# Performance work log

Hardware: AMD Instinct MI355X
Metric: run time of the kernel (lower is better)

Reference implementation:

```python
import jax, jax.numpy as jnp
import numpy as np

D_MODEL = 1024
N_HEAD = 16
HEAD_DIM = D_MODEL // N_HEAD
D_FF = 4096
N_EXPERTS = 4
EPS = 1e-05


def _layer_norm(x, gamma, beta):
    mu = jnp.mean(x, axis=-1, keepdims=True)
    var = jnp.mean((x - mu) ** 2, axis=-1, keepdims=True)
    return (x - mu) / jnp.sqrt(var + EPS) * gamma + beta


def setup_inputs() -> dict:
    key = jax.random.key(0)
    ks = jax.random.split(key, 20)
    f32 = jnp.float32
    sc = 1.0 / np.sqrt(D_MODEL)
    scf = 1.0 / np.sqrt(D_FF)
    return {
        "src": jax.random.normal(ks[0], (4, 512, D_MODEL), f32),
        "Wq": jax.random.normal(ks[1], (D_MODEL, D_MODEL), f32) * sc,
        "bq": jnp.zeros((D_MODEL,), f32),
        "Wk": jax.random.normal(ks[2], (D_MODEL, D_MODEL), f32) * sc,
        "bk": jnp.zeros((D_MODEL,), f32),
        "Wv": jax.random.normal(ks[3], (D_MODEL, D_MODEL), f32) * sc,
        "bv": jnp.zeros((D_MODEL,), f32),
        "Wo": jax.random.normal(ks[4], (D_MODEL, D_MODEL), f32) * sc,
        "bo": jnp.zeros((D_MODEL,), f32),
        "router_w": jax.random.normal(ks[5], (D_MODEL, 1), f32) * 0.05,
        "router_b": jnp.zeros((1,), f32),
        "W1": jax.random.normal(ks[6], (N_EXPERTS, D_MODEL, D_FF), f32) * sc,
        "b1": jnp.zeros((N_EXPERTS, D_FF), f32),
        "W2": jax.random.normal(ks[7], (N_EXPERTS, D_FF, D_MODEL), f32) * scf,
        "b2": jnp.zeros((N_EXPERTS, D_MODEL), f32),
        "ln1_g": jnp.ones((D_MODEL,), f32),
        "ln1_b": jnp.zeros((D_MODEL,), f32),
        "ln2_g": jnp.ones((D_MODEL,), f32),
        "ln2_b": jnp.zeros((D_MODEL,), f32),
    }


def reference(src, Wq, bq, Wk, bk, Wv, bv, Wo, bo, router_w, router_b,
              W1, b1, W2, b2, ln1_g, ln1_b, ln2_g, ln2_b):
    B, T, _ = src.shape
    # --- self attention ---
    q = (src @ Wq + bq).reshape(B, T, N_HEAD, HEAD_DIM)
    k = (src @ Wk + bk).reshape(B, T, N_HEAD, HEAD_DIM)
    v = (src @ Wv + bv).reshape(B, T, N_HEAD, HEAD_DIM)
    scale = HEAD_DIM ** -0.5
    scores = jnp.einsum('bqhd,bkhd->bhqk', q, k) * scale
    probs = jax.nn.softmax(scores, axis=-1)
    attn = jnp.einsum('bhqk,bkhd->bqhd', probs, v).reshape(B, T, D_MODEL)
    attn = attn @ Wo + bo
    x = _layer_norm(src + attn, ln1_g, ln1_b)
    # --- hash-routed single-expert MoE FFN ---
    keys = (x @ router_w + router_b)[..., 0]           # [B, T]
    expert_idx = jnp.remainder(jnp.floor(keys).astype(jnp.int32), N_EXPERTS)
    ff_out = jnp.zeros_like(x)
    for e in range(N_EXPERTS):
        h = jax.nn.relu(x @ W1[e] + b1[e])             # [B, T, D_FF]
        y = h @ W2[e] + b2[e]                          # [B, T, D_MODEL]
        ff_out = ff_out + jnp.where((expert_idx == e)[..., None], y, 0.0)
    return _layer_norm(x + ff_out, ln2_g, ln2_b)
```

## Files before the change

kernel.cpp:

```cpp
#include <hip/hip_runtime.h>
#include <hip/hip_bf16.h>
#include <stdint.h>

typedef unsigned short u16;
typedef __attribute__((ext_vector_type(8))) short s8v;
typedef __attribute__((ext_vector_type(4))) float f4v;

#define DEVI static __device__ __forceinline__

DEVI u16 f2bf(float x) {
  union { float f; unsigned u; } a; a.f = x;
  return (u16)((a.u + 0x7fffu + ((a.u >> 16) & 1u)) >> 16);
}
DEVI float bf2f(u16 h) {
  union { float f; unsigned u; } a; a.u = ((unsigned)h) << 16; return a.f;
}
DEVI float wred_add(float s) {
#pragma unroll
  for (int o = 32; o; o >>= 1) s += __shfl_xor(s, o, 64);
  return s;
}
DEVI f4v mfma16(s8v a, s8v b, f4v c) {
  return __builtin_amdgcn_mfma_f32_16x16x32_bf16(a, b, c, 0, 0, 0);
}

DEVI int rho(int j) { return ((j & 12) << 1) | (j & 3) | ((j >> 4) << 2); }

DEVI void gload16(const u16* gp, u16* lp) {
  __builtin_amdgcn_global_load_lds(
      (const __attribute__((address_space(1))) uint32_t*)gp,
      (__attribute__((address_space(3))) uint32_t*)lp, 16, 0, 0);
}

DEVI s8v ldfrag_sw(const u16* base, int r, int lg) {
  int off = ((r >> 4) << 9) + ((r & 15) << 5) + ((lg ^ ((r >> 1) & 3)) << 3);
  return *(const s8v*)(base + off);
}

template<bool LO>
DEVI void tsplit_body(const float* __restrict__ in, u16* __restrict__ outH, u16* __restrict__ outL,
                      int cc, int rr, int R, int C, float (*t)[132], int id) {
#pragma unroll
  for (int i = 0; i < 4; ++i) {
    int slot = i * 256 + id;
    int r = slot >> 5, c4 = slot & 31;
    float4 v = *(const float4*)&in[(long long)(rr + r) * C + cc + c4 * 4];
    *(float4*)&t[r + (r >> 2)][c4 * 4] = v;
  }
  __syncthreads();
#pragma unroll
  for (int i = 0; i < 4; ++i) {
    int slot = i * 256 + id;
    int j = slot >> 3, gs = slot & 7;
    int s0 = 5 * gs;
    float v0 = t[s0 + 0][j], v1 = t[s0 + 1][j], v2 = t[s0 + 2][j], v3 = t[s0 + 3][j];
    long long o = (long long)(cc + j) * R + rr + 8 * (gs & 3) + 4 * (gs >> 2);
    ushort4 hv;
    hv.x = f2bf(v0); hv.y = f2bf(v1); hv.z = f2bf(v2); hv.w = f2bf(v3);
    *(ushort4*)&outH[o] = hv;
    if (LO) {
      ushort4 lv;
      lv.x = f2bf(v0 - bf2f(hv.x)); lv.y = f2bf(v1 - bf2f(hv.y));
      lv.z = f2bf(v2 - bf2f(hv.z)); lv.w = f2bf(v3 - bf2f(hv.w));
      *(ushort4*)&outL[o] = lv;
    }
  }
}

__global__ __launch_bounds__(256) void prep1_k(const float* __restrict__ src,
    const float* __restrict__ Wq, const float* __restrict__ Wk,
    const float* __restrict__ Wv, const float* __restrict__ Wo,
    const float* __restrict__ bq, const float* __restrict__ bk, const float* __restrict__ bv,
    u16* __restrict__ srcH, u16* __restrict__ srcL,
    u16* __restrict__ WqkvTh, u16* __restrict__ WqkvTl,
    u16* __restrict__ WoTh, u16* __restrict__ WoTl, float* __restrict__ bqkv) {
  __shared__ float tbuf[39][132];
  const int bid = blockIdx.x, tid = threadIdx.x;
  if (bid < 2048) {
    int i = bid * 256 + tid;
    float4 v = ((const float4*)src)[i];
    ushort4 hv, lv;
    hv.x = f2bf(v.x); lv.x = f2bf(v.x - bf2f(hv.x));
    hv.y = f2bf(v.y); lv.y = f2bf(v.y - bf2f(hv.y));
    hv.z = f2bf(v.z); lv.z = f2bf(v.z - bf2f(hv.z));
    hv.w = f2bf(v.w); lv.w = f2bf(v.w - bf2f(hv.w));
    int t = i & 7, blk = i >> 3;
    int si = blk * 8 + ((t & 3) << 1) + (t >> 2);
    ((ushort4*)srcH)[si] = hv;
    ((ushort4*)srcL)[si] = lv;
  } else if (bid < 3072) {
    int t = bid - 2048;
    int wsel = t >> 8, tb = t & 255;
    const float* in = wsel == 0 ? Wq : wsel == 1 ? Wk : wsel == 2 ? Wv : Wo;
    u16* oh = wsel < 3 ? WqkvTh + wsel * 1024 * 1024 : WoTh;
    u16* ol = wsel < 3 ? WqkvTl + wsel * 1024 * 1024 : WoTl;
    tsplit_body<true>(in, oh, ol, (tb & 7) * 128, (tb >> 3) * 32, 1024, 1024, tbuf, tid);
  } else {
    int i = (bid - 3072) * 256 + tid;
    bqkv[i] = i < 1024 ? bq[i] : (i < 2048 ? bk[i - 1024] : bv[i - 2048]);
  }
}

__global__ __launch_bounds__(256) void prep2_k(const float* __restrict__ W1, const float* __restrict__ W2,
                                               u16* __restrict__ W1T, u16* __restrict__ W2T) {
  __shared__ float tbuf[39][132];
  const int bid = blockIdx.x, tid = threadIdx.x;
  if (bid < 4096) {
    int bx = bid & 31, by = (bid >> 5) & 31, bz = bid >> 10;
    tsplit_body<false>(W1 + (long long)bz * 1024 * 4096, W1T + (long long)bz * 4096 * 1024, nullptr,
                       bx * 128, by * 32, 1024, 4096, tbuf, tid);
  } else {
    int t = bid - 4096;
    int bx = t & 7, by = (t >> 3) & 127, bz = t >> 10;
    tsplit_body<false>(W2 + (long long)bz * 4096 * 1024, W2T + (long long)bz * 1024 * 4096, nullptr,
                       bx * 128, by * 32, 4096, 1024, tbuf, tid);
  }
}

__global__ __launch_bounds__(256) void transpose_pair_k(const u16* __restrict__ inH, const u16* __restrict__ inL,
                                                        u16* __restrict__ oH, u16* __restrict__ oL) {
  __shared__ u16 th[32][40], tl[32][40];
  const int b = blockIdx.z;
  const int dd = blockIdx.x * 32;
  const int tt = blockIdx.y * 32;
  const int id = threadIdx.y * 32 + threadIdx.x;
  const int rr = id >> 3, g = id & 7;
  const int rg = 8 * (g & 3) + 4 * (g >> 2);
  const int64_t ibase = ((int64_t)(b * 512 + tt)) * 3072 + 2048 + dd;
  ushort4 hv = *(const ushort4*)&inH[ibase + (int64_t)rr * 3072 + rg];
  ushort4 lv = *(const ushort4*)&inL[ibase + (int64_t)rr * 3072 + rg];
  *(ushort4*)&th[rr][4 * g] = hv;
  *(ushort4*)&tl[rr][4 * g] = lv;
  __syncthreads();
  const int j = rr;
  ushort4 ho, lo;
  ho.x = th[4 * g + 0][j]; ho.y = th[4 * g + 1][j]; ho.z = th[4 * g + 2][j]; ho.w = th[4 * g + 3][j];
  lo.x = tl[4 * g + 0][j]; lo.y = tl[4 * g + 1][j]; lo.z = tl[4 * g + 2][j]; lo.w = tl[4 * g + 3][j];
  const int64_t obase = ((int64_t)b * 1024 + dd + j) * 512 + tt + rg;
  *(ushort4*)&oH[obase] = ho;
  *(ushort4*)&oL[obase] = lo;
}

__global__ __launch_bounds__(512, 2) void attn_sm_k(const u16* __restrict__ qkvH,
                                                    const u16* __restrict__ qkvL,
                                                    u16* __restrict__ probs) {
  __shared__ __align__(16) u16 sK[2][16384];
  __shared__ __align__(16) float smax[128][4];
  __shared__ __align__(16) float ssum[128][4];
  const int tid = threadIdx.x;
  const int w = tid >> 6, lane = tid & 63;
  const int wq = w >> 2, wt = w & 3;
  const int lr = lane & 15, lg = lane >> 4;
  const int bx = blockIdx.x, bh = blockIdx.y;
  const int64_t tokBase = (int64_t)(bh >> 4) * 512;
  const int h = bh & 15;
  const int qcol = h * 64, kcol = 1024 + h * 64;
  const int srow = lane >> 2;
  const int sG = (lane & 3) ^ ((lane >> 3) & 3);

#pragma unroll
  for (int c = 0; c < 8; ++c) {
    int s = c * 8 + w;
    int ks = s >> 5, rb = s & 31;
    int64_t go = (tokBase + rb * 16 + srow) * 3072 + kcol + ks * 32 + sG * 8;
    gload16(qkvH + go, &sK[ks][rb * 512]);
  }
  __syncthreads();

  f4v acc[4][8];
#pragma unroll
  for (int mi = 0; mi < 4; ++mi)
#pragma unroll
    for (int ni = 0; ni < 8; ++ni) acc[mi][ni] = f4v{0.f, 0.f, 0.f, 0.f};

#pragma unroll
  for (int ks = 0; ks < 2; ++ks) {
    s8v ah[4], al[4];
#pragma unroll
    for (int mi = 0; mi < 4; ++mi) {
      int64_t tok = tokBase + bx * 128 + wq * 64 + mi * 16 + lr;
      const u16* p = qkvH + tok * 3072 + qcol + ks * 32 + lg * 8;
      ah[mi] = *(const s8v*)p;
      al[mi] = *(const s8v*)(qkvL + (p - qkvH));
    }
#pragma unroll
    for (int ni = 0; ni < 8; ++ni) {
      int r = wt * 128 + ni * 16 + lr;
      s8v bh_ = ldfrag_sw(&sK[ks][0], r, lg);
      s8v bl_ = *(const s8v*)(qkvL + (tokBase + r) * 3072 + kcol + ks * 32 + lg * 8);
#pragma unroll
      for (int mi = 0; mi < 4; ++mi) {
        acc[mi][ni] = mfma16(ah[mi], bh_, acc[mi][ni]);
        acc[mi][ni] = mfma16(ah[mi], bl_, acc[mi][ni]);
        acc[mi][ni] = mfma16(al[mi], bh_, acc[mi][ni]);
      }
    }
  }

#pragma unroll
  for (int mi = 0; mi < 4; ++mi)
#pragma unroll
    for (int ni = 0; ni < 8; ++ni) {
      acc[mi][ni][0] *= 0.125f; acc[mi][ni][1] *= 0.125f;
      acc[mi][ni][2] *= 0.125f; acc[mi][ni][3] *= 0.125f;
    }

  float rm[4][4];
#pragma unroll
  for (int mi = 0; mi < 4; ++mi)
#pragma unroll
    for (int j = 0; j < 4; ++j) {
      float m = acc[mi][0][j];
#pragma unroll
      for (int ni = 1; ni < 8; ++ni) m = fmaxf(m, acc[mi][ni][j]);
#pragma unroll
      for (int o = 1; o < 16; o <<= 1) m = fmaxf(m, __shfl_xor(m, o, 64));
      rm[mi][j] = m;
    }
  if (lr == 0) {
#pragma unroll
    for (int mi = 0; mi < 4; ++mi)
#pragma unroll
      for (int j = 0; j < 4; ++j)
        smax[wq * 64 + mi * 16 + lg * 4 + j][wt] = rm[mi][j];
  }
  __syncthreads();
  float mrow[4][4];
#pragma unroll
  for (int mi = 0; mi < 4; ++mi)
#pragma unroll
    for (int j = 0; j < 4; ++j) {
      float4 t4 = *(const float4*)&smax[wq * 64 + mi * 16 + lg * 4 + j][0];
      mrow[mi][j] = fmaxf(fmaxf(t4.x, t4.y), fmaxf(t4.z, t4.w));
    }

  float rs_[4][4];
#pragma unroll
  for (int mi = 0; mi < 4; ++mi)
#pragma unroll
    for (int j = 0; j < 4; ++j) {
      float s = 0.f;
#pragma unroll
      for (int ni = 0; ni < 8; ++ni) {
        float e = expf(acc[mi][ni][j] - mrow[mi][j]);
        acc[mi][ni][j] = e;
        s += e;
      }
#pragma unroll
      for (int o = 1; o < 16; o <<= 1) s += __shfl_xor(s, o, 64);
      rs_[mi][j] = s;
    }
  if (lr == 0) {
#pragma unroll
    for (int mi = 0; mi < 4; ++mi)
#pragma unroll
      for (int j = 0; j < 4; ++j)
        ssum[wq * 64 + mi * 16 + lg * 4 + j][wt] = rs_[mi][j];
  }
  __syncthreads();

#pragma unroll
  for (int mi = 0; mi < 4; ++mi)
#pragma unroll
    for (int j = 0; j < 4; ++j) {
      int row = wq * 64 + mi * 16 + lg * 4 + j;
      float4 t4 = *(const float4*)&ssum[row][0];
      float inv = 1.f / (((t4.x + t4.y) + t4.z) + t4.w);
      u16* rp = probs + ((int64_t)bh * 512 + bx * 128 + row) * 1024;
#pragma unroll
      for (int ni = 0; ni < 8; ++ni) {
        int tcol = wt * 128 + ni * 16 + lr;
        int cs = (tcol & ~31) | rho(tcol & 31);
        float p = acc[mi][ni][j] * inv;
        u16 hv = f2bf(p);
        rp[cs] = hv;
        rp[512 + cs] = f2bf(p - bf2f(hv));
      }
    }
}

struct GemmArgs {
  const u16* Ah; const u16* Al; int lda;
  const u16* Bh; const u16* Bl; int ldb;
  float* C; u16* Ch; u16* Cl; int ldc;
  const float* bias;
  int K;
  int Z2;
  int64_t aZ1, aZ2, bZ1, bZ2, cZ1, cZ2;
  const int* ofs;
  int64_t bStrE; int biasStrE;
  int NX, NY, YG;
};

template<int BM, int BN, bool SPLIT, int EPI, bool PN, int MINW, bool SWZ>
__global__ __launch_bounds__(256, MINW) void gemm_k(GemmArgs g) {
  constexpr int ASZ = BM * 32, BSZ = BN * 32;
  constexpr int AN = SPLIT ? 2 * ASZ : ASZ;
  constexpr int BNT = SPLIT ? 2 * BSZ : BSZ;
  constexpr int nA = BM / 16, nB = BN / 16;
  constexpr int nAt = SPLIT ? 2 * nA : nA;
  constexpr int TOT = nAt + (SPLIT ? 2 * nB : nB);
  static_assert(TOT % 4 == 0, "chunk count must divide across 4 waves");
  constexpr int NLOAD = TOT / 4;
  __shared__ __align__(16) u16 sA[2][AN];
  __shared__ __align__(16) u16 sB[2][BNT];

  const int tid = threadIdx.x;
  int bx, by, bz;
  if (SWZ) {
    const int nwg = gridDim.x;
    int wg = (blockIdx.x & 7) * (nwg >> 3) + (blockIdx.x >> 3);
    int byl = wg % g.YG; int t = wg / g.YG;
    bx = t % g.NX; t /= g.NX;
    const int nyg = g.NY / g.YG;
    by = (t % nyg) * g.YG + byl;
    bz = t / nyg;
  } else {
    bx = blockIdx.x; by = blockIdx.y; bz = blockIdx.z;
  }

  const u16* Ah = g.Ah; const u16* Al = g.Al;
  const u16* Bh = g.Bh; const u16* Bl = g.Bl;
  int64_t cOff = 0;
  if (g.Z2 > 0) {
    int z1 = bz / g.Z2, z2 = bz % g.Z2;
    int64_t ao = (int64_t)z1 * g.aZ1 + (int64_t)z2 * g.aZ2;
    int64_t bo = (int64_t)z1 * g.bZ1 + (int64_t)z2 * g.bZ2;
    Ah += ao; Bh += bo;
    if (SPLIT) { Al += ao; Bl += bo; }
    cOff = (int64_t)z1 * g.cZ1 + (int64_t)z2 * g.cZ2;
  }
  const int row0 = bx * BM;
  const int col0 = by * BN;
  const float* bias = g.bias;
  if (g.ofs) {
    if (row0 >= g.ofs[4]) return;
    int e = 0;
    while (e < 3 && row0 >= g.ofs[e + 1]) ++e;
    Bh += (int64_t)e * g.bStrE;
    if (bias) bias += (int64_t)e * g.biasStrE;
  }

  const int w = tid >> 6, lane = tid & 63;
  const int wr = w >> 1, wc = w & 1;
  const int lr = lane & 15, lg = lane >> 4;
  constexpr int FM = BM / 32, FN = BN / 32;

  const int srow = lane >> 2;
  const int sG = (lane & 3) ^ ((lane >> 3) & 3);

  auto stage = [&](int b, int kt) {
#pragma unroll
    for (int c = 0; c < NLOAD; ++c) {
      int s = c * 4 + w;
      if (s < nA) {
        int64_t go = (int64_t)(row0 + s * 16 + srow) * g.lda + kt + sG * 8;
        gload16(Ah + go, &sA[b][s * 512]);
      } else if (SPLIT && s < 2 * nA) {
        int ch = s - nA;
        int64_t go = (int64_t)(row0 + ch * 16 + srow) * g.lda + kt + sG * 8;
        gload16(Al + go, &sA[b][ASZ + ch * 512]);
      } else if (s < nAt + nB) {
        int ch = s - nAt;
        int64_t go = (int64_t)(col0 + ch * 16 + srow) * g.ldb + kt + sG * 8;
        gload16(Bh + go, &sB[b][ch * 512]);
      } else {
        int ch = s - nAt - nB;
        int64_t go = (int64_t)(col0 + ch * 16 + srow) * g.ldb + kt + sG * 8;
        gload16(Bl + go, &sB[b][BSZ + ch * 512]);
      }
    }
  };

  f4v acc[FM][FN];
#pragma unroll
  for (int i = 0; i < FM; ++i)
#pragma unroll
    for (int j = 0; j < FN; ++j) acc[i][j] = f4v{0.f, 0.f, 0.f, 0.f};

  s8v a0[FM], b0[FN], al0[SPLIT ? FM : 1], bl0[SPLIT ? FN : 1];
  s8v a1[FM], b1[FN], al1[SPLIT ? FM : 1], bl1[SPLIT ? FN : 1];

  auto rdfrags = [&](int buf, auto& af, auto& bf, auto& afl, auto& bfl) {
#pragma unroll
    for (int mi = 0; mi < FM; ++mi) {
      int r = wr * (BM / 2) + mi * 16 + lr;
      af[mi] = ldfrag_sw(&sA[buf][0], r, lg);
      if (SPLIT) afl[mi] = ldfrag_sw(&sA[buf][ASZ], r, lg);
    }
#pragma unroll
    for (int ni = 0; ni < FN; ++ni) {
      int r = wc * (BN / 2) + ni * 16 + lr;
      bf[ni] = ldfrag_sw(&sB[buf][0], r, lg);
      if (SPLIT) bfl[ni] = ldfrag_sw(&sB[buf][BSZ], r, lg);
    }
  };

  const int nt = g.K >> 5;

  stage(0, 0);
  stage(1, 32);
  asm volatile("s_waitcnt vmcnt(%0)" :: "n"(NLOAD) : "memory");
  __builtin_amdgcn_sched_barrier(0);
  __builtin_amdgcn_s_barrier();
  rdfrags(0, a0, b0, al0, bl0);

  auto body = [&](int t, auto& cA, auto& cB, auto& cAl, auto& cBl,
                  auto& nA_, auto& nB_, auto& nAl_, auto& nBl_) {
    asm volatile("s_waitcnt lgkmcnt(0)" ::: "memory");
    __builtin_amdgcn_sched_barrier(0);
    __builtin_amdgcn_s_barrier();
    if (t + 2 < nt) stage(t & 1, (t + 2) << 5);
    if (t + 1 < nt) {
      if (t + 2 < nt)
        asm volatile("s_waitcnt vmcnt(%0)" :: "n"(NLOAD) : "memory");
      else
        asm volatile("s_waitcnt vmcnt(0)" ::: "memory");
      __builtin_amdgcn_sched_barrier(0);
      __builtin_amdgcn_s_barrier();
      rdfrags((t + 1) & 1, nA_, nB_, nAl_, nBl_);
    }
    __builtin_amdgcn_sched_barrier(0);
    __builtin_amdgcn_s_setprio(1);
#pragma unroll
    for (int mi = 0; mi < FM; ++mi)
#pragma unroll
      for (int ni = 0; ni < FN; ++ni) {
        acc[mi][ni] = mfma16(cA[mi], cB[ni], acc[mi][ni]);
        if (SPLIT) {
          acc[mi][ni] = mfma16(cA[mi], cBl[ni], acc[mi][ni]);
          acc[mi][ni] = mfma16(cAl[mi], cB[ni], acc[mi][ni]);
        }
      }
    __builtin_amdgcn_s_setprio(0);
  };

  for (int t = 0; t < nt; t += 2) {
    body(t,     a0, b0, al0, bl0, a1, b1, al1, bl1);
    body(t + 1, a1, b1, al1, bl1, a0, b0, al0, bl0);
  }

#pragma unroll
  for (int mi = 0; mi < FM; ++mi) {
    int rbase = row0 + wr * (BM / 2) + mi * 16 + lg * 4;
#pragma unroll
    for (int ni = 0; ni < FN; ++ni) {
      int c = col0 + wc * (BN / 2) + ni * 16 + lr;
      int cs = PN ? ((c & ~31) | rho(c & 31)) : c;
      float bv = bias ? bias[c] : 0.f;
#pragma unroll
      for (int j = 0; j < 4; ++j) {
        int r = rbase + j;
        float v = acc[mi][ni][j] + bv;
        if (EPI == 0) {
          g.C[cOff + (int64_t)r * g.ldc + cs] = v;
        } else if (EPI == 1) {
          u16 h = f2bf(v);
          int64_t o = cOff + (int64_t)r * g.ldc + cs;
          g.Ch[o] = h;
          g.Cl[o] = f2bf(v - bf2f(h));
        } else {
          v = v > 0.f ? v : 0.f;
          g.Ch[cOff + (int64_t)r * g.ldc + cs] = f2bf(v);
        }
      }
    }
  }
}

__global__ __launch_bounds__(256) void ln_router_k(const float* __restrict__ a, const float* __restrict__ b,
                                                   const float* __restrict__ gm, const float* __restrict__ bt,
                                                   const float* __restrict__ rw, const float* __restrict__ rb,
                                                   float* __restrict__ out, int* __restrict__ eidx) {
  __shared__ float sm[4];
  const int r = blockIdx.x, tid = threadIdx.x;
  const int w = tid >> 6, lane = tid & 63;
  float4 va = ((const float4*)(a + (int64_t)r * 1024))[tid];
  float4 vb = ((const float4*)(b + (int64_t)r * 1024))[tid];
  float x0 = va.x + vb.x, x1 = va.y + vb.y, x2 = va.z + vb.z, x3 = va.w + vb.w;
  float s = wred_add(x0 + x1 + x2 + x3);
  if (lane == 0) sm[w] = s;
  __syncthreads();
  float mu = (sm[0] + sm[1] + sm[2] + sm[3]) * (1.f / 1024.f);
  float d0 = x0 - mu, d1 = x1 - mu, d2 = x2 - mu, d3 = x3 - mu;
  float q = wred_add(d0 * d0 + d1 * d1 + d2 * d2 + d3 * d3);
  __syncthreads();
  if (lane == 0) sm[w] = q;
  __syncthreads();
  float var = (sm[0] + sm[1] + sm[2] + sm[3]) * (1.f / 1024.f);
  float rs = 1.f / sqrtf(var + 1e-5f);
  float4 g4 = ((const float4*)gm)[tid];
  float4 b4 = ((const float4*)bt)[tid];
  float4 o;
  o.x = d0 * rs * g4.x + b4.x;
  o.y = d1 * rs * g4.y + b4.y;
  o.z = d2 * rs * g4.z + b4.z;
  o.w = d3 * rs * g4.w + b4.w;
  ((float4*)(out + (int64_t)r * 1024))[tid] = o;
  float4 w4 = ((const float4*)rw)[tid];
  float p = o.x * w4.x + o.y * w4.y + o.z * w4.z + o.w * w4.w;
  p = wred_add(p);
  __syncthreads();
  if (lane == 0) sm[w] = p;
  __syncthreads();
  if (tid == 0) {
    float key = (sm[0] + sm[1] + sm[2] + sm[3]) + rb[0];
    eidx[r] = (int)floorf(key) & 3;
  }
}

__global__ __launch_bounds__(256) void reduce_ln_k(const float* __restrict__ part, const int* __restrict__ rowsrc,
                                                   const int* __restrict__ ofs, const float* __restrict__ b2,
                                                   const float* __restrict__ xb, const float* __restrict__ gm,
                                                   const float* __restrict__ bt, float* __restrict__ out) {
  __shared__ float sm[4];
  const int r = blockIdx.x;
  if (r >= ofs[4]) return;
  const int s = rowsrc[r];
  if (s < 0) return;
  int e = 0;
  while (e < 3 && r >= ofs[e + 1]) ++e;
  const int tid = threadIdx.x, w = tid >> 6, lane = tid & 63;
  const int64_t RN = 2560ll * 1024;
  float4 v0 = ((const float4*)(part + 0 * RN + (int64_t)r * 1024))[tid];
  float4 v1 = ((const float4*)(part + 1 * RN + (int64_t)r * 1024))[tid];
  float4 v2 = ((const float4*)(part + 2 * RN + (int64_t)r * 1024))[tid];
  float4 v3 = ((const float4*)(part + 3 * RN + (int64_t)r * 1024))[tid];
  float4 bb = ((const float4*)(b2 + (int64_t)e * 1024))[tid];
  float4 va = ((const float4*)(xb + (int64_t)s * 1024))[tid];
  float y0 = ((v0.x + v1.x) + v2.x) + v3.x + bb.x;
  float y1 = ((v0.y + v1.y) + v2.y) + v3.y + bb.y;
  float y2 = ((v0.z + v1.z) + v2.z) + v3.z + bb.z;
  float y3 = ((v0.w + v1.w) + v2.w) + v3.w + bb.w;
  float x0 = va.x + y0, x1 = va.y + y1, x2 = va.z + y2, x3 = va.w + y3;
  float sum = wred_add(x0 + x1 + x2 + x3);
  if (lane == 0) sm[w] = sum;
  __syncthreads();
  float mu = (sm[0] + sm[1] + sm[2] + sm[3]) * (1.f / 1024.f);
  float d0 = x0 - mu, d1 = x1 - mu, d2 = x2 - mu, d3 = x3 - mu;
  float q = wred_add(d0 * d0 + d1 * d1 + d2 * d2 + d3 * d3);
  __syncthreads();
  if (lane == 0) sm[w] = q;
  __syncthreads();
  float var = (sm[0] + sm[1] + sm[2] + sm[3]) * (1.f / 1024.f);
  float rs = 1.f / sqrtf(var + 1e-5f);
  float4 g4 = ((const float4*)gm)[tid];
  float4 b4 = ((const float4*)bt)[tid];
  float4 o;
  o.x = d0 * rs * g4.x + b4.x;
  o.y = d1 * rs * g4.y + b4.y;
  o.z = d2 * rs * g4.z + b4.z;
  o.w = d3 * rs * g4.w + b4.w;
  ((float4*)(out + (int64_t)s * 1024))[tid] = o;
}

__global__ __launch_bounds__(256) void compact_k(const int* __restrict__ eidx,
                                                 int* __restrict__ rowsrc, int* __restrict__ ofs) {
  __shared__ unsigned long long sc[256];
  __shared__ int soff[5];
  const int tid = threadIdx.x;
  int myE[8];
  unsigned long long c = 0;
#pragma unroll
  for (int i = 0; i < 8; ++i) {
    int e = eidx[tid * 8 + i];
    myE[i] = e;
    c += 1ull << (e * 16);
  }
  sc[tid] = c;
  __syncthreads();
  for (int o = 1; o < 256; o <<= 1) {
    unsigned long long v = (tid >= o) ? sc[tid - o] : 0ull;
    __syncthreads();
    sc[tid] += v;
    __syncthreads();
  }
  unsigned long long incl = sc[tid], tot = sc[255];
  unsigned long long excl = incl - c;
  if (tid == 0) {
    int off = 0;
    for (int e = 0; e < 4; ++e) {
      soff[e] = off;
      int cnt = (int)((tot >> (e * 16)) & 0xffff);
      off += (cnt + 127) & ~127;
    }
    soff[4] = off;
    for (int e = 0; e < 5; ++e) ofs[e] = soff[e];
  }
  __syncthreads();
  for (int r = tid; r < 2560; r += 256) rowsrc[r] = -1;
  __threadfence_block();
  __syncthreads();
  int rank[4];
#pragma unroll
  for (int e = 0; e < 4; ++e) rank[e] = (int)((excl >> (e * 16)) & 0xffff);
#pragma unroll
  for (int i = 0; i < 8; ++i) {
    int e = myE[i];
    rowsrc[soff[e] + rank[e]] = tid * 8 + i;
    rank[e]++;
  }
}

__global__ __launch_bounds__(256) void gather_k(const float* __restrict__ x, const int* __restrict__ rowsrc,
                                                const int* __restrict__ ofs, u16* __restrict__ xg) {
  int r = blockIdx.x;
  if (r >= ofs[4]) return;
  int s = rowsrc[r];
  int c = threadIdx.x;
  float4 v = (s >= 0) ? ((const float4*)(x + (int64_t)s * 1024))[c] : float4{0.f, 0.f, 0.f, 0.f};
  ushort4 o;
  o.x = f2bf(v.x); o.y = f2bf(v.y); o.z = f2bf(v.z); o.w = f2bf(v.w);
  int t = c & 7, blk = c >> 3;
  int si = blk * 8 + ((t & 3) << 1) + (t >> 2);
  ((ushort4*)(xg + (int64_t)r * 1024))[si] = o;
}

extern "C" void kernel_launch(void* const* d_in, const int* in_sizes, int n_in,
                              void* d_out, int out_size, void* d_ws, size_t ws_size,
                              hipStream_t stream) {
  const float* src = (const float*)d_in[0];
  const float* Wq  = (const float*)d_in[1];
  const float* bq  = (const float*)d_in[2];
  const float* Wk  = (const float*)d_in[3];
  const float* bk  = (const float*)d_in[4];
  const float* Wv  = (const float*)d_in[5];
  const float* bv  = (const float*)d_in[6];
  const float* Wo  = (const float*)d_in[7];
  const float* bo  = (const float*)d_in[8];
  const float* rw  = (const float*)d_in[9];
  const float* rb  = (const float*)d_in[10];
  const float* W1  = (const float*)d_in[11];
  const float* b1  = (const float*)d_in[12];
  const float* W2  = (const float*)d_in[13];
  const float* b2  = (const float*)d_in[14];
  const float* g1  = (const float*)d_in[15];
  const float* be1 = (const float*)d_in[16];
  const float* g2  = (const float*)d_in[17];
  const float* be2 = (const float*)d_in[18];
  float* out = (float*)d_out;

  char* base = (char*)d_ws;
  size_t off = 0;
  auto alloc = [&](size_t bytes) -> char* {
    char* p = base + off;
    off += (bytes + 255) & ~(size_t)255;
    return p;
  };
  const size_t MB = 1ull << 20;
  u16* srcH = (u16*)alloc(4 * MB);
  u16* srcL = (u16*)alloc(4 * MB);
  u16* WqkvTh = (u16*)alloc(6 * MB);
  u16* WqkvTl = (u16*)alloc(6 * MB);
  u16* WoTh = (u16*)alloc(2 * MB);
  u16* WoTl = (u16*)alloc(2 * MB);
  float* bqkv = (float*)alloc(16 * 1024);
  u16* qkvH = (u16*)alloc(12 * MB);
  u16* qkvL = (u16*)alloc(12 * MB);
  u16* hbuf = (u16*)qkvH;
  u16* vTH = (u16*)alloc(4 * MB); u16* vTL = (u16*)alloc(4 * MB);
  float* scores = (float*)alloc(64 * MB);
  u16* W1T = (u16*)scores;
  u16* W2T = (u16*)scores + 16ull * 1024 * 1024;
  u16* attnH = (u16*)alloc(4 * MB); u16* attnL = (u16*)alloc(4 * MB);
  u16* xg = (u16*)attnH;
  float* woOut = (float*)alloc(8 * MB);
  float* xbuf = (float*)alloc(8 * MB);
  float* partials = (float*)alloc(40 * MB);
  int* eidx   = (int*)alloc(2048 * 4);
  int* rowsrc = (int*)alloc(2560 * 4);
  int* ofs    = (int*)alloc(32);
  (void)ws_size; (void)in_sizes; (void)n_in; (void)out_size;

  dim3 tb(32, 8);

  prep1_k<<<3084, 256, 0, stream>>>(src, Wq, Wk, Wv, Wo, bq, bk, bv,
                                    srcH, srcL, WqkvTh, WqkvTl, WoTh, WoTl, bqkv);

  {
    GemmArgs g{};
    g.Ah = srcH; g.Al = srcL; g.lda = 1024;
    g.Bh = WqkvTh; g.Bl = WqkvTl; g.ldb = 1024;
    g.Ch = qkvH; g.Cl = qkvL; g.ldc = 3072;
    g.bias = bqkv; g.K = 1024; g.Z2 = 0;
    g.NX = 16; g.NY = 32; g.YG = 8;
    gemm_k<128, 96, true, 1, true, 2, true><<<dim3(512), 256, 0, stream>>>(g);
  }
  transpose_pair_k<<<dim3(32, 16, 4), tb, 0, stream>>>(qkvH, qkvL, vTH, vTL);

  attn_sm_k<<<dim3(4, 64), 512, 0, stream>>>(qkvH, qkvL, (u16*)scores);

  {
    GemmArgs g{};
    g.Ah = (const u16*)scores; g.Al = (const u16*)scores + 512; g.lda = 1024;
    g.Bh = vTH; g.Bl = vTL; g.ldb = 512;
    g.Ch = attnH; g.Cl = attnL; g.ldc = 1024;
    g.K = 512; g.Z2 = 16;
    g.aZ1 = 16ll * 512 * 1024; g.aZ2 = 512ll * 1024;
    g.bZ1 = 1024ll * 512;      g.bZ2 = 64ll * 512;
    g.cZ1 = 512ll * 1024;      g.cZ2 = 64;
    gemm_k<64, 64, true, 1, true, 3, false><<<dim3(8, 1, 64), 256, 0, stream>>>(g);
  }
  {
    GemmArgs g{};
    g.Ah = attnH; g.Al = attnL; g.lda = 1024;
    g.Bh = WoTh; g.Bl = WoTl; g.ldb = 1024;
    g.C = woOut; g.ldc = 1024;
    g.bias = bo; g.K = 1024; g.Z2 = 0;
    gemm_k<64, 64, true, 0, false, 3, false><<<dim3(32, 16, 1), 256, 0, stream>>>(g);
  }
  ln_router_k<<<2048, 256, 0, stream>>>(src, woOut, g1, be1, rw, rb, xbuf, eidx);

  compact_k<<<1, 256, 0, stream>>>(eidx, rowsrc, ofs);
  gather_k<<<2560, 256, 0, stream>>>(xbuf, rowsrc, ofs, xg);

  prep2_k<<<8192, 256, 0, stream>>>(W1, W2, W1T, W2T);

  {
    GemmArgs g{};
    g.Ah = xg; g.lda = 1024;
    g.Bh = W1T; g.ldb = 1024;
    g.Ch = hbuf; g.ldc = 4096;
    g.bias = b1; g.biasStrE = 4096;
    g.K = 1024; g.Z2 = 0;
    g.ofs = ofs; g.bStrE = 4096ll * 1024;
    g.NX = 20; g.NY = 32; g.YG = 16;
    gemm_k<128, 128, false, 2, true, 3, true><<<dim3(640), 256, 0, stream>>>(g);
  }
  {
    GemmArgs g{};
    g.Ah = hbuf; g.lda = 4096;
    g.Bh = W2T; g.ldb = 4096;
    g.C = partials; g.ldc = 1024;
    g.bias = nullptr;
    g.K = 1024; g.Z2 = 4;
    g.aZ1 = 0; g.aZ2 = 1024;
    g.bZ1 = 0; g.bZ2 = 1024;
    g.cZ1 = 0; g.cZ2 = 2560ll * 1024;
    g.ofs = ofs; g.bStrE = 4096ll * 1024;
    g.NX = 20; g.NY = 8; g.YG = 8;
    gemm_k<128, 128, false, 0, false, 3, true><<<dim3(640), 256, 0, stream>>>(g);
  }
  reduce_ln_k<<<2560, 256, 0, stream>>>(partials, rowsrc, ofs, b2, xbuf, g2, be2, out);
}
```

Baseline: 272.5 us.

## Load GEMM A fragments directly from global into registers, bypass LDS

```diff
diff --git a/kernel.cpp b/kernel.cpp
--- a/kernel.cpp
+++ b/kernel.cpp
@@ -294,15 +294,15 @@
 
 template<int BM, int BN, bool SPLIT, int EPI, bool PN, int MINW, bool SWZ>
 __global__ __launch_bounds__(256, MINW) void gemm_k(GemmArgs g) {
-  constexpr int ASZ = BM * 32, BSZ = BN * 32;
-  constexpr int AN = SPLIT ? 2 * ASZ : ASZ;
+  constexpr int BSZ = BN * 32;
   constexpr int BNT = SPLIT ? 2 * BSZ : BSZ;
-  constexpr int nA = BM / 16, nB = BN / 16;
-  constexpr int nAt = SPLIT ? 2 * nA : nA;
-  constexpr int TOT = nAt + (SPLIT ? 2 * nB : nB);
-  static_assert(TOT % 4 == 0, "chunk count must divide across 4 waves");
-  constexpr int NLOAD = TOT / 4;
-  __shared__ __align__(16) u16 sA[2][AN];
+  constexpr int nB = BN / 16;
+  constexpr int CH = SPLIT ? 2 * nB : nB;
+  static_assert(CH % 4 == 0, "B chunk count must divide across 4 waves");
+  constexpr int NLOADB = CH / 4;
+  constexpr int FM = BM / 32, FN = BN / 32;
+  constexpr int AF = SPLIT ? 2 * FM : FM;
+  constexpr int KW = NLOADB + AF;
   __shared__ __align__(16) u16 sB[2][BNT];
 
   const int tid = threadIdx.x;
@@ -344,28 +344,20 @@
   const int w = tid >> 6, lane = tid & 63;
   const int wr = w >> 1, wc = w & 1;
   const int lr = lane & 15, lg = lane >> 4;
-  constexpr int FM = BM / 32, FN = BN / 32;
 
   const int srow = lane >> 2;
   const int sG = (lane & 3) ^ ((lane >> 3) & 3);
 
-  auto stage = [&](int b, int kt) {
-#pragma unroll
-    for (int c = 0; c < NLOAD; ++c) {
+  auto stageB = [&](int b, int kt) {
+#pragma unroll
+    for (int c = 0; c < NLOADB; ++c) {
       int s = c * 4 + w;
-      if (s < nA) {
-        int64_t go = (int64_t)(row0 + s * 16 + srow) * g.lda + kt + sG * 8;
-        gload16(Ah + go, &sA[b][s * 512]);
-      } else if (SPLIT && s < 2 * nA) {
-        int ch = s - nA;
-        int64_t go = (int64_t)(row0 + ch * 16 + srow) * g.lda + kt + sG * 8;
-        gload16(Al + go, &sA[b][ASZ + ch * 512]);
-      } else if (s < nAt + nB) {
-        int ch = s - nAt;
+      if (!SPLIT || s < nB) {
+        int ch = s;
         int64_t go = (int64_t)(col0 + ch * 16 + srow) * g.ldb + kt + sG * 8;
         gload16(Bh + go, &sB[b][ch * 512]);
       } else {
-        int ch = s - nAt - nB;
+        int ch = s - nB;
         int64_t go = (int64_t)(col0 + ch * 16 + srow) * g.ldb + kt + sG * 8;
         gload16(Bl + go, &sB[b][BSZ + ch * 512]);
       }
@@ -381,13 +373,15 @@
   s8v a0[FM], b0[FN], al0[SPLIT ? FM : 1], bl0[SPLIT ? FN : 1];
   s8v a1[FM], b1[FN], al1[SPLIT ? FM : 1], bl1[SPLIT ? FN : 1];
 
-  auto rdfrags = [&](int buf, auto& af, auto& bf, auto& afl, auto& bfl) {
+  auto rdA = [&](int kt, auto& af, auto& afl) {
 #pragma unroll
     for (int mi = 0; mi < FM; ++mi) {
-      int r = wr * (BM / 2) + mi * 16 + lr;
-      af[mi] = ldfrag_sw(&sA[buf][0], r, lg);
-      if (SPLIT) afl[mi] = ldfrag_sw(&sA[buf][ASZ], r, lg);
-    }
+      int64_t ro = (int64_t)(row0 + wr * (BM / 2) + mi * 16 + lr) * g.lda + kt + lg * 8;
+      af[mi] = *(const s8v*)(Ah + ro);
+      if (SPLIT) afl[mi] = *(const s8v*)(Al + ro);
+    }
+  };
+  auto rdB = [&](int buf, auto& bf, auto& bfl) {
 #pragma unroll
     for (int ni = 0; ni < FN; ++ni) {
       int r = wc * (BN / 2) + ni * 16 + lr;
@@ -398,27 +392,29 @@
 
   const int nt = g.K >> 5;
 
-  stage(0, 0);
-  stage(1, 32);
-  asm volatile("s_waitcnt vmcnt(%0)" :: "n"(NLOAD) : "memory");
+  stageB(0, 0);
+  stageB(1, 32);
+  rdA(0, a0, al0);
+  asm volatile("s_waitcnt vmcnt(%0)" :: "n"(KW) : "memory");
   __builtin_amdgcn_sched_barrier(0);
   __builtin_amdgcn_s_barrier();
-  rdfrags(0, a0, b0, al0, bl0);
+  rdB(0, b0, bl0);
 
   auto body = [&](int t, auto& cA, auto& cB, auto& cAl, auto& cBl,
                   auto& nA_, auto& nB_, auto& nAl_, auto& nBl_) {
     asm volatile("s_waitcnt lgkmcnt(0)" ::: "memory");
     __builtin_amdgcn_sched_barrier(0);
     __builtin_amdgcn_s_barrier();
-    if (t + 2 < nt) stage(t & 1, (t + 2) << 5);
+    if (t + 2 < nt) stageB(t & 1, (t + 2) << 5);
     if (t + 1 < nt) {
       if (t + 2 < nt)
-        asm volatile("s_waitcnt vmcnt(%0)" :: "n"(NLOAD) : "memory");
+        asm volatile("s_waitcnt vmcnt(%0)" :: "n"(KW) : "memory");
       else
         asm volatile("s_waitcnt vmcnt(0)" ::: "memory");
       __builtin_amdgcn_sched_barrier(0);
       __builtin_amdgcn_s_barrier();
-      rdfrags((t + 1) & 1, nA_, nB_, nAl_, nBl_);
+      rdA((t + 1) << 5, nA_, nAl_);
+      rdB((t + 1) & 1, nB_, nBl_);
     }
     __builtin_amdgcn_sched_barrier(0);
     __builtin_amdgcn_s_setprio(1);
@@ -684,7 +680,7 @@
     g.Ch = qkvH; g.Cl = qkvL; g.ldc = 3072;
     g.bias = bqkv; g.K = 1024; g.Z2 = 0;
     g.NX = 16; g.NY = 32; g.YG = 8;
-    gemm_k<128, 96, true, 1, true, 2, true><<<dim3(512), 256, 0, stream>>>(g);
+    gemm_k<128, 96, true, 1, true, 3, true><<<dim3(512), 256, 0, stream>>>(g);
   }
   transpose_pair_k<<<dim3(32, 16, 4), tb, 0, stream>>>(qkvH, qkvL, vTH, vTL);
 
```

Result: slower. 465.2 us (+70.7%).
